# Kernel tuning notes

Measured on AMD Instinct MI355X. Metric: run time of the kernel, lower is better.

## Reference

```python
import jax, jax.numpy as jnp
import numpy as np

K = 20
EPS = 1e-5
NEG_SLOPE = 0.2


def _knn_idx(x, k):
    # x: (B, N, C). Torch: pd = -||xi||^2 + 2 xi.xj - ||xj||^2, topk largest = nearest.
    inner = jnp.einsum('bnc,bmc->bnm', x, x)
    xx = jnp.sum(x * x, axis=-1)  # (B, N)
    pd = 2.0 * inner - xx[:, :, None] - xx[:, None, :]
    _, idx = jax.lax.top_k(pd, k)  # (B, N, k)
    return idx


def _bn_lrelu(h, gamma, beta, axes):
    mean = jnp.mean(h, axis=axes)
    var = jnp.var(h, axis=axes)  # biased, as in torch BN training normalization
    hn = (h - mean) * jax.lax.rsqrt(var + EPS) * gamma + beta
    return jnp.where(hn >= 0, hn, NEG_SLOPE * hn)


def _edge_conv(x, W, gamma, beta, k):
    # x: (B, N, C); W: (O, 2C). Returns (B, N, O).
    idx = _knn_idx(x, k)
    nbr = jax.vmap(lambda xb, ib: xb[ib])(x, idx)  # (B, N, k, C) gather
    center = jnp.broadcast_to(x[:, :, None, :], nbr.shape)
    edge = jnp.concatenate([nbr - center, center], axis=-1)  # (B, N, k, 2C)
    h = jnp.einsum('bnkc,oc->bnko', edge, W)
    h = _bn_lrelu(h, gamma, beta, axes=(0, 1, 2))
    return jnp.max(h, axis=2)  # max over k -> (B, N, O)


def setup_inputs() -> dict:
    key = jax.random.key(0)
    ks = jax.random.split(key, 16)
    B, N = 32, 1024
    d = {'x': jax.random.normal(ks[0], (B, N, 3), dtype=jnp.float32)}
    dims = [(64, 6), (64, 128), (128, 128), (256, 256), (1024, 512)]
    for i, (o, c) in enumerate(dims, start=1):
        d[f'W{i}'] = jax.random.normal(ks[i], (o, c), dtype=jnp.float32) * 0.05
        d[f'g{i}'] = jnp.ones((o,), dtype=jnp.float32)
        d[f'b{i}'] = jnp.zeros((o,), dtype=jnp.float32)
    return d


def reference(x, W1, g1, b1, W2, g2, b2, W3, g3, b3, W4, g4, b4, W5, g5, b5):
    B = x.shape[0]
    x1 = _edge_conv(x, W1, g1, b1, K)    # (B, N, 64)
    x2 = _edge_conv(x1, W2, g2, b2, K)   # (B, N, 64)
    x3 = _edge_conv(x2, W3, g3, b3, K)   # (B, N, 128)
    x4 = _edge_conv(x3, W4, g4, b4, K)   # (B, N, 256)
    cat = jnp.concatenate([x1, x2, x3, x4], axis=-1)  # (B, N, 512)
    h = jnp.einsum('bnc,oc->bno', cat, W5)            # (B, N, 1024)
    h = _bn_lrelu(h, g5, b5, axes=(0, 1))
    out = jnp.max(h, axis=1)  # adaptive max pool over points -> (B, 1024)
    return out.reshape(B, 1, -1)
```

## Files before the change

kernel.cpp:

```cpp
#include <hip/hip_runtime.h>
#include <math.h>

#define BB 32
#define NN 1024
#define KNNK 20
#define PTS (BB*NN)

typedef __attribute__((ext_vector_type(8)))  short short8;
typedef __attribute__((ext_vector_type(4)))  float f32x4;
typedef __attribute__((ext_vector_type(16))) float f32x16;

__device__ __forceinline__ float lrelu(float v){ return v >= 0.f ? v : 0.2f*v; }

__device__ __forceinline__ unsigned short f2b(float x){
    union { float f; unsigned u; } c; c.f = x;
    unsigned r = c.u + 0x7FFFu + ((c.u >> 16) & 1u);
    return (unsigned short)(r >> 16);
}

__global__ void sq_kernel(const float* __restrict__ x, int stride, int C, float* __restrict__ xx){
    int pn = blockIdx.x*256 + threadIdx.x;
    if (pn >= PTS) return;
    const float* r = x + (size_t)pn*stride;
    float s = 0.f;
    for (int c = 0; c < C; ++c){ float v = r[c]; s = fmaf(v, v, s); }
    xx[pn] = s;
}

template<int C>
__global__ void __launch_bounds__(256) dist_kernel(const float* __restrict__ x, int stride,
                                                   const float* __restrict__ xx,
                                                   float* __restrict__ D, int b0){
    constexpr int KC = (C < 32 ? C : 32);
    __shared__ float As[KC][132];
    __shared__ float Bs[KC][132];
    const int tid = threadIdx.x;
    int t = blockIdx.x, ti = 0;
    while (t >= 8 - ti){ t -= 8 - ti; ++ti; }
    const int tj = ti + t;
    const int i0 = ti*128, j0 = tj*128;
    const int bl = blockIdx.z;
    const int b  = b0 + bl;
    const float* xb = x + (size_t)b*NN*stride;
    const int rt = tid >> 4, ct = tid & 15;
    float acc[8][8] = {{0.f}};

    for (int kc = 0; kc < C; kc += KC){
        __syncthreads();
        if constexpr (KC % 4 == 0){
            for (int i = tid; i < 128*(KC/4); i += 256){
                int kq = i % (KC/4), rr = i / (KC/4);
                float4 va = *(const float4*)&xb[(size_t)(i0+rr)*stride + kc + kq*4];
                As[kq*4+0][rr]=va.x; As[kq*4+1][rr]=va.y; As[kq*4+2][rr]=va.z; As[kq*4+3][rr]=va.w;
                float4 vb = *(const float4*)&xb[(size_t)(j0+rr)*stride + kc + kq*4];
                Bs[kq*4+0][rr]=vb.x; Bs[kq*4+1][rr]=vb.y; Bs[kq*4+2][rr]=vb.z; Bs[kq*4+3][rr]=vb.w;
            }
        } else {
            for (int i = tid; i < 128*KC; i += 256){
                int k = i % KC, rr = i / KC;
                As[k][rr] = xb[(size_t)(i0+rr)*stride + kc + k];
                Bs[k][rr] = xb[(size_t)(j0+rr)*stride + kc + k];
            }
        }
        __syncthreads();
        #pragma unroll
        for (int k = 0; k < KC; ++k){
            float4 a0 = *(const float4*)&As[k][rt*8];
            float4 a1 = *(const float4*)&As[k][rt*8+4];
            float4 b0v= *(const float4*)&Bs[k][ct*8];
            float4 b1v= *(const float4*)&Bs[k][ct*8+4];
            float av[8]={a0.x,a0.y,a0.z,a0.w,a1.x,a1.y,a1.z,a1.w};
            float bw[8]={b0v.x,b0v.y,b0v.z,b0v.w,b1v.x,b1v.y,b1v.z,b1v.w};
            #pragma unroll
            for (int i = 0; i < 8; ++i)
                #pragma unroll
                for (int j = 0; j < 8; ++j)
                    acc[i][j] = fmaf(av[i], bw[j], acc[i][j]);
        }
    }
    const float* xxb = xx + b*NN;
    float xi[8], xj[8];
    #pragma unroll
    for (int i=0;i<8;++i) xi[i] = xxb[i0 + rt*8 + i];
    #pragma unroll
    for (int j=0;j<8;++j) xj[j] = xxb[j0 + ct*8 + j];
    #pragma unroll
    for (int i=0;i<8;++i){
        float4 d0, d1;
        d0.x = 2.f*acc[i][0] - xi[i] - xj[0];
        d0.y = 2.f*acc[i][1] - xi[i] - xj[1];
        d0.z = 2.f*acc[i][2] - xi[i] - xj[2];
        d0.w = 2.f*acc[i][3] - xi[i] - xj[3];
        d1.x = 2.f*acc[i][4] - xi[i] - xj[4];
        d1.y = 2.f*acc[i][5] - xi[i] - xj[5];
        d1.z = 2.f*acc[i][6] - xi[i] - xj[6];
        d1.w = 2.f*acc[i][7] - xi[i] - xj[7];
        float* drow = &D[((size_t)bl*NN + i0 + rt*8 + i)*NN + j0 + ct*8];
        *(float4*)drow = d0;
        *(float4*)(drow+4) = d1;
    }
    if (ti != tj){
        #pragma unroll
        for (int j=0;j<8;++j){
            float4 m0, m1;
            m0.x = 2.f*acc[0][j] - xj[j] - xi[0];
            m0.y = 2.f*acc[1][j] - xj[j] - xi[1];
            m0.z = 2.f*acc[2][j] - xj[j] - xi[2];
            m0.w = 2.f*acc[3][j] - xj[j] - xi[3];
            m1.x = 2.f*acc[4][j] - xj[j] - xi[4];
            m1.y = 2.f*acc[5][j] - xj[j] - xi[5];
            m1.z = 2.f*acc[6][j] - xj[j] - xi[6];
            m1.w = 2.f*acc[7][j] - xj[j] - xi[7];
            float* mrow = &D[((size_t)bl*NN + j0 + ct*8 + j)*NN + i0 + rt*8];
            *(float4*)mrow = m0;
            *(float4*)(mrow+4) = m1;
        }
    }
}

__global__ void __launch_bounds__(256) topk_kernel(const float* __restrict__ D,
                                                   int* __restrict__ idxout, int baseRow){
    const int tid = threadIdx.x;
    const int wv = tid >> 6, lane = tid & 63;
    const int rid = blockIdx.x*4 + wv;
    const float* drow = D + (size_t)rid * NN;
    unsigned u[16];
    #pragma unroll
    for (int i = 0; i < 16; ++i){
        unsigned bits = __float_as_uint(drow[i*64 + lane]);
        unsigned m = (bits & 0x80000000u) ? 0xFFFFFFFFu : 0x80000000u;
        u[i] = bits ^ m;
    }
    unsigned t = 0u;
    for (int b = 31; b >= 0; --b){
        unsigned cand = t | (1u << b);
        int cnt = 0;
        #pragma unroll
        for (int i = 0; i < 16; ++i)
            cnt += (int)__popcll(__ballot(u[i] >= cand));
        if (cnt >= KNNK) t = cand;
    }
    const unsigned long long lt = (lane == 0) ? 0ull : ((~0ull) >> (64 - lane));
    int* orow = idxout + ((size_t)baseRow + rid) * KNNK;
    int cbase = 0;
    #pragma unroll
    for (int i = 0; i < 16; ++i){
        bool gt2 = (u[i] > t);
        unsigned long long mask = __ballot(gt2);
        if (gt2) orow[cbase + (int)__popcll(mask & lt)] = i*64 + lane;
        cbase += (int)__popcll(mask);
    }
    #pragma unroll
    for (int i = 0; i < 16; ++i){
        bool eq = (u[i] == t);
        unsigned long long mask = __ballot(eq);
        int pos = cbase + (int)__popcll(mask & lt);
        if (eq && pos < KNNK) orow[pos] = i*64 + lane;
        cbase += (int)__popcll(mask);
    }
}

template<int C, int O>
__global__ void __launch_bounds__(256) gemmG_kernel(const float* __restrict__ x, int stride,
                                                    const float* __restrict__ W,
                                                    float* __restrict__ G1, float* __restrict__ Gd){
    constexpr int KC = (C < 32 ? C : 32);
    __shared__ float Xl [KC][68];
    __shared__ float W1l[KC][68];
    __shared__ float W2l[KC][68];
    const int tid = threadIdx.x;
    const int r0 = blockIdx.x * 64;
    const int o0 = blockIdx.y * 64;
    const int rt = tid & 15, ct = tid >> 4;

    float a1[4][4] = {{0.f}}, a2[4][4] = {{0.f}};
    for (int kc = 0; kc < C; kc += KC){
        __syncthreads();
        for (int i = tid; i < KC*64; i += 256){
            int k = i % KC, rr = i / KC;
            Xl [k][rr] = x[(size_t)(r0+rr)*stride + kc + k];
            W1l[k][rr] = W[(size_t)(o0+rr)*(2*C) + kc + k];
            W2l[k][rr] = W[(size_t)(o0+rr)*(2*C) + C + kc + k];
        }
        __syncthreads();
        #pragma unroll
        for (int k = 0; k < KC; ++k){
            float4 xa = *(const float4*)&Xl [k][rt*4];
            float4 w1 = *(const float4*)&W1l[k][ct*4];
            float4 w2 = *(const float4*)&W2l[k][ct*4];
            float xv[4] = {xa.x, xa.y, xa.z, xa.w};
            #pragma unroll
            for (int i = 0; i < 4; ++i){
                a1[i][0] = fmaf(xv[i], w1.x, a1[i][0]);
                a1[i][1] = fmaf(xv[i], w1.y, a1[i][1]);
                a1[i][2] = fmaf(xv[i], w1.z, a1[i][2]);
                a1[i][3] = fmaf(xv[i], w1.w, a1[i][3]);
                a2[i][0] = fmaf(xv[i], w2.x, a2[i][0]);
                a2[i][1] = fmaf(xv[i], w2.y, a2[i][1]);
                a2[i][2] = fmaf(xv[i], w2.z, a2[i][2]);
                a2[i][3] = fmaf(xv[i], w2.w, a2[i][3]);
            }
        }
    }
    #pragma unroll
    for (int i = 0; i < 4; ++i){
        size_t row = (size_t)(r0 + rt*4 + i);
        float4 g1v = make_float4(a1[i][0], a1[i][1], a1[i][2], a1[i][3]);
        float4 gdv = make_float4(a2[i][0]-a1[i][0], a2[i][1]-a1[i][1],
                                 a2[i][2]-a1[i][2], a2[i][3]-a1[i][3]);
        *(float4*)&G1[row*O + o0 + ct*4] = g1v;
        *(float4*)&Gd[row*O + o0 + ct*4] = gdv;
    }
}

template<int O>
__global__ void __launch_bounds__(256) gather_kernel(const float* __restrict__ G1,
                                                     const float* __restrict__ Gd,
                                                     const int* __restrict__ idxg, int bgbase,
                                                     float* __restrict__ catslice,
                                                     float* __restrict__ stats){
    constexpr int OG = O/4;
    constexpr int PP = 256/OG;
    constexpr int NP = 16;
    __shared__ int nbs[NP][KNNK];
    const int nwg = (int)gridDim.x;
    int bid = (int)blockIdx.x;
    if ((nwg & 7) == 0){
        const int cpx = nwg >> 3;
        bid = (bid & 7) * cpx + (bid >> 3);
    }
    const int tid = threadIdx.x;
    const int p0 = bid * NP;
    for (int i = tid; i < NP*KNNK; i += 256){
        int pp = i / KNNK, kk = i - pp*KNNK;
        int pl = p0 + pp;
        nbs[pp][kk] = ((pl >> 10) << 10) + idxg[(size_t)(bgbase + pl)*KNNK + kk];
    }
    __syncthreads();
    const int o4 = (tid % OG)*4;
    const int pq = tid / OG;
    float S1[4] = {0.f,0.f,0.f,0.f}, S2[4] = {0.f,0.f,0.f,0.f};
    for (int pp = pq; pp < NP; pp += PP){
        int pl = p0 + pp;
        float4 dv = *(const float4*)&Gd[(size_t)pl*O + o4];
        float d[4] = {dv.x, dv.y, dv.z, dv.w};
        float mx[4] = {-INFINITY,-INFINITY,-INFINITY,-INFINITY};
        float ls[4] = {0.f,0.f,0.f,0.f}, lq[4] = {0.f,0.f,0.f,0.f};
        #pragma unroll
        for (int kk = 0; kk < KNNK; ++kk){
            float4 gv = *(const float4*)&G1[(size_t)nbs[pp][kk]*O + o4];
            float ga[4] = {gv.x, gv.y, gv.z, gv.w};
            #pragma unroll
            for (int c = 0; c < 4; ++c){
                mx[c] = fmaxf(mx[c], ga[c]);
                ls[c] += ga[c];
                lq[c] = fmaf(ga[c], ga[c], lq[c]);
            }
        }
        float4 outv;
        float* op = &outv.x;
        #pragma unroll
        for (int c = 0; c < 4; ++c){
            S1[c] += ls[c] + 20.f*d[c];
            S2[c] += lq[c] + 2.f*d[c]*ls[c] + 20.f*d[c]*d[c];
            op[c] = mx[c] + d[c];
        }
        *(float4*)&catslice[(size_t)(bgbase + pl)*512 + o4] = outv;
    }
    int rep = bid & 63;
    #pragma unroll
    for (int c = 0; c < 4; ++c){
        atomicAdd(&stats[rep*2*O + o4 + c],     S1[c]);
        atomicAdd(&stats[rep*2*O + O + o4 + c], S2[c]);
    }
}

__global__ void fin_kernel(const float* __restrict__ stats, int O, float cnt,
                           float* __restrict__ mean, float* __restrict__ invstd){
    int o = threadIdx.x;
    if (o >= O) return;
    float s1 = 0.f, s2 = 0.f;
    for (int r = 0; r < 64; ++r){
        s1 += stats[r*2*O + o];
        s2 += stats[r*2*O + O + o];
    }
    float m = s1 / cnt;
    float v = s2 / cnt - m*m;
    mean[o] = m;
    invstd[o] = rsqrtf(v + 1e-5f);
}

template<int O>
__global__ void apply_kernel(float* __restrict__ catslice,
                             const float* __restrict__ mean, const float* __restrict__ invstd,
                             const float* __restrict__ g, const float* __restrict__ bt){
    int i = blockIdx.x*256 + threadIdx.x;
    int pn = i / O, o = i - pn*O;
    float* p = &catslice[(size_t)pn*512 + o];
    float hn = (*p - mean[o]) * invstd[o] * g[o] + bt[o];
    *p = lrelu(hn);
}

__global__ void tob16_kernel(const float* __restrict__ src, unsigned short* __restrict__ dst, int n4){
    int i = blockIdx.x*256 + threadIdx.x;
    if (i >= n4) return;
    float4 v = *(const float4*)&src[(size_t)i*4];
    ushort4 o;
    o.x = f2b(v.x); o.y = f2b(v.y); o.z = f2b(v.z); o.w = f2b(v.w);
    *(ushort4*)&dst[(size_t)i*4] = o;
}

__global__ void __launch_bounds__(256) l5m_kernel(const unsigned short* __restrict__ Am,
                                                  const unsigned short* __restrict__ Bm,
                                                  float* __restrict__ pmax,
                                                  float* __restrict__ psum,
                                                  float* __restrict__ psq){
    __shared__ __align__(16) unsigned short As[128][64];
    __shared__ __align__(16) unsigned short Bs[128][64];
    const int tid = threadIdx.x;
    const int r0 = blockIdx.x * 128;
    const int o0 = blockIdx.y * 128;
    const int w = tid >> 6, lane = tid & 63;
    const int m32 = lane & 31, kh = lane >> 5;
    const int wm = (w & 1) * 64;
    const int wn = (w >> 1) * 64;

    f32x16 acc[2][2];
    #pragma unroll
    for (int i=0;i<2;++i)
        #pragma unroll
        for (int j=0;j<2;++j)
            #pragma unroll
            for (int r=0;r<16;++r) acc[i][j][r] = 0.f;

    for (int kc = 0; kc < 512; kc += 64){
        __syncthreads();
        #pragma unroll
        for (int t = 0; t < 4; ++t){
            int i = tid + t*256;
            int rr = i >> 3, ch = i & 7;
            int sl = ch ^ (rr & 7);
            *(uint4*)&As[rr][sl*8] = *(const uint4*)&Am[(size_t)(r0+rr)*512 + kc + ch*8];
            *(uint4*)&Bs[rr][sl*8] = *(const uint4*)&Bm[(size_t)(o0+rr)*512 + kc + ch*8];
        }
        __syncthreads();
        #pragma unroll
        for (int q = 0; q < 4; ++q){
            int lk = q*2 + kh;
            short8 a[2], bfr[2];
            #pragma unroll
            for (int mb = 0; mb < 2; ++mb){
                int rA = wm + mb*32 + m32;
                a[mb] = *(const short8*)&As[rA][(lk ^ (rA & 7))*8];
            }
            #pragma unroll
            for (int nb = 0; nb < 2; ++nb){
                int rB = wn + nb*32 + m32;
                bfr[nb] = *(const short8*)&Bs[rB][(lk ^ (rB & 7))*8];
            }
            #pragma unroll
            for (int mb = 0; mb < 2; ++mb)
                #pragma unroll
                for (int nb = 0; nb < 2; ++nb)
                    acc[mb][nb] = __builtin_amdgcn_mfma_f32_32x32x16_bf16(a[mb], bfr[nb], acc[mb][nb], 0, 0, 0);
        }
    }
    __syncthreads();
    float* red = (float*)&As[0][0];
    #pragma unroll
    for (int nb = 0; nb < 2; ++nb){
        float mx = -INFINITY, s1 = 0.f, s2 = 0.f;
        #pragma unroll
        for (int mb = 0; mb < 2; ++mb)
            #pragma unroll
            for (int r = 0; r < 16; ++r){
                float v = acc[mb][nb][r];
                mx = fmaxf(mx, v); s1 += v; s2 = fmaf(v, v, s2);
            }
        mx = fmaxf(mx, __shfl_xor(mx, 32));
        s1 += __shfl_xor(s1, 32);
        s2 += __shfl_xor(s2, 32);
        if (lane < 32){
            int col = wn + nb*32 + m32;
            float* p = red + ((size_t)(w & 1) * 128 + col) * 3;
            p[0] = mx; p[1] = s1; p[2] = s2;
        }
    }
    __syncthreads();
    if (tid < 128){
        const float* p0 = red + (size_t)tid*3;
        const float* p1 = red + (size_t)(128 + tid)*3;
        float mx = fmaxf(p0[0], p1[0]);
        float s1 = p0[1] + p1[1];
        float s2 = p0[2] + p1[2];
        size_t pi = (size_t)blockIdx.x*1024 + o0 + tid;
        pmax[pi] = mx; psum[pi] = s1; psq[pi] = s2;
    }
}

__global__ void fin5_kernel(const float* __restrict__ pmax, const float* __restrict__ psum,
                            const float* __restrict__ psq,
                            const float* __restrict__ g, const float* __restrict__ bt,
                            float* __restrict__ out){
    int o = blockIdx.x*256 + threadIdx.x;
    float s1 = 0.f, s2 = 0.f;
    for (int r = 0; r < 256; ++r){
        s1 += psum[(size_t)r*1024 + o];
        s2 += psq [(size_t)r*1024 + o];
    }
    float m  = s1 / 32768.f;
    float v  = s2 / 32768.f - m*m;
    float is = rsqrtf(v + 1e-5f);
    float gg = g[o], bb2 = bt[o];
    for (int b = 0; b < 32; ++b){
        float mx = -INFINITY;
        #pragma unroll
        for (int ns = 0; ns < 8; ++ns) mx = fmaxf(mx, pmax[((size_t)b*8 + ns)*1024 + o]);
        float hn = (mx - m) * is * gg + bb2;
        out[(size_t)b*1024 + o] = lrelu(hn);
    }
}

extern "C" void kernel_launch(void* const* d_in, const int* in_sizes, int n_in,
                              void* d_out, int out_size, void* d_ws, size_t ws_size,
                              hipStream_t stream) {
    (void)in_sizes; (void)n_in; (void)out_size;
    const float* x  = (const float*)d_in[0];
    const float* W1 = (const float*)d_in[1];  const float* g1 = (const float*)d_in[2];  const float* b1 = (const float*)d_in[3];
    const float* W2 = (const float*)d_in[4];  const float* g2 = (const float*)d_in[5];  const float* b2 = (const float*)d_in[6];
    const float* W3 = (const float*)d_in[7];  const float* g3 = (const float*)d_in[8];  const float* b3 = (const float*)d_in[9];
    const float* W4 = (const float*)d_in[10]; const float* g4 = (const float*)d_in[11]; const float* b4 = (const float*)d_in[12];
    const float* W5 = (const float*)d_in[13]; const float* g5 = (const float*)d_in[14]; const float* b5 = (const float*)d_in[15];
    float* out = (float*)d_out;

    const size_t fixedBytes = (size_t)PTS*512*4 + (size_t)PTS*KNNK*4 + (size_t)PTS*4
                            + (size_t)64*2*256*4 + 2048*4 + 3*(size_t)256*1024*4
                            + (size_t)1024*512*2;
    int CB;
    if      (ws_size >= fixedBytes + (size_t)32*NN*NN*4) CB = 32;
    else if (ws_size >= fixedBytes + (size_t)16*NN*NN*4) CB = 16;
    else                                                 CB = 8;
    const size_t Rbytes = (size_t)CB*NN*NN*4;

    char* wsp = (char*)d_ws;
    float* cat    = (float*)wsp; wsp += (size_t)PTS*512*4;
    char*  R      = wsp;         wsp += Rbytes;
    int*   idx    = (int*)  wsp; wsp += (size_t)PTS*KNNK*4;
    float* xx     = (float*)wsp; wsp += (size_t)PTS*4;
    float* stats  = (float*)wsp; wsp += (size_t)64*2*256*4;
    float* mean   = (float*)wsp; wsp += 1024*4;
    float* invstd = (float*)wsp; wsp += 1024*4;
    float* pmax   = (float*)wsp; wsp += (size_t)256*1024*4;
    float* psum   = (float*)wsp; wsp += (size_t)256*1024*4;
    float* psq    = (float*)wsp; wsp += (size_t)256*1024*4;
    unsigned short* W5b = (unsigned short*)wsp; wsp += (size_t)1024*512*2;

    float* Dbuf  = (float*)R;
    float* G1    = (float*)R;
    float* GdS   = (float*)(R + (size_t)16*1024*1024);
    float* GdB   = (float*)(R + (size_t)32*1024*1024);
    unsigned short* catB = (unsigned short*)R;

    const float cntE = (float)(PTS*KNNK);
    const int nch = 32 / CB;
    const bool bigG = (Rbytes >= (size_t)64*1024*1024);

    sq_kernel<<<PTS/256, 256, 0, stream>>>(x, 3, 3, xx);
    for (int bc = 0; bc < nch; ++bc){
        dist_kernel<3><<<dim3(36,1,CB), 256, 0, stream>>>(x, 3, xx, Dbuf, bc*CB);
        topk_kernel<<<CB*1024/4, 256, 0, stream>>>(Dbuf, idx, bc*CB*1024);
    }
    hipMemsetAsync(stats, 0, 64*2*256*4, stream);
    gemmG_kernel<3,64><<<dim3(512,1), 256, 0, stream>>>(x, 3, W1, G1, GdS);
    gather_kernel<64><<<2048, 256, 0, stream>>>(G1, GdS, idx, 0, cat + 0, stats);
    fin_kernel<<<1, 64, 0, stream>>>(stats, 64, cntE, mean, invstd);
    apply_kernel<64><<<PTS*64/256, 256, 0, stream>>>(cat + 0, mean, invstd, g1, b1);

    sq_kernel<<<PTS/256, 256, 0, stream>>>(cat + 0, 512, 64, xx);
    for (int bc = 0; bc < nch; ++bc){
        dist_kernel<64><<<dim3(36,1,CB), 256, 0, stream>>>(cat + 0, 512, xx, Dbuf, bc*CB);
        topk_kernel<<<CB*1024/4, 256, 0, stream>>>(Dbuf, idx, bc*CB*1024);
    }
    hipMemsetAsync(stats, 0, 64*2*256*4, stream);
    gemmG_kernel<64,64><<<dim3(512,1), 256, 0, stream>>>(cat + 0, 512, W2, G1, GdS);
    gather_kernel<64><<<2048, 256, 0, stream>>>(G1, GdS, idx, 0, cat + 64, stats);
    fin_kernel<<<1, 64, 0, stream>>>(stats, 64, cntE, mean, invstd);
    apply_kernel<64><<<PTS*64/256, 256, 0, stream>>>(cat + 64, mean, invstd, g2, b2);

    sq_kernel<<<PTS/256, 256, 0, stream>>>(cat + 64, 512, 64, xx);
    for (int bc = 0; bc < nch; ++bc){
        dist_kernel<64><<<dim3(36,1,CB), 256, 0, stream>>>(cat + 64, 512, xx, Dbuf, bc*CB);
        topk_kernel<<<CB*1024/4, 256, 0, stream>>>(Dbuf, idx, bc*CB*1024);
    }
    hipMemsetAsync(stats, 0, 64*2*256*4, stream);
    gemmG_kernel<64,128><<<dim3(512,2), 256, 0, stream>>>(cat + 64, 512, W3, G1, GdS);
    gather_kernel<128><<<2048, 256, 0, stream>>>(G1, GdS, idx, 0, cat + 128, stats);
    fin_kernel<<<1, 128, 0, stream>>>(stats, 128, cntE, mean, invstd);
    apply_kernel<128><<<PTS*128/256, 256, 0, stream>>>(cat + 128, mean, invstd, g3, b3);

    sq_kernel<<<PTS/256, 256, 0, stream>>>(cat + 128, 512, 128, xx);
    for (int bc = 0; bc < nch; ++bc){
        dist_kernel<128><<<dim3(36,1,CB), 256, 0, stream>>>(cat + 128, 512, xx, Dbuf, bc*CB);
        topk_kernel<<<CB*1024/4, 256, 0, stream>>>(Dbuf, idx, bc*CB*1024);
    }
    hipMemsetAsync(stats, 0, 64*2*256*4, stream);
    if (bigG){
        gemmG_kernel<128,256><<<dim3(512,4), 256, 0, stream>>>(cat + 128, 512, W4, G1, GdB);
        gather_kernel<256><<<2048, 256, 0, stream>>>(G1, GdB, idx, 0, cat + 256, stats);
    } else {
        for (int bg = 0; bg < 4; ++bg){
            gemmG_kernel<128,256><<<dim3(128,4), 256, 0, stream>>>(cat + 128 + (size_t)bg*8192*512, 512, W4, G1, GdS);
            gather_kernel<256><<<512, 256, 0, stream>>>(G1, GdS, idx, bg*8192, cat + 256, stats);
        }
    }
    fin_kernel<<<1, 256, 0, stream>>>(stats, 256, cntE, mean, invstd);
    apply_kernel<256><<<PTS*256/256, 256, 0, stream>>>(cat + 256, mean, invstd, g4, b4);

    tob16_kernel<<<PTS*512/4/256, 256, 0, stream>>>(cat, catB, PTS*512/4);
    tob16_kernel<<<1024*512/4/256, 256, 0, stream>>>(W5, W5b, 1024*512/4);
    l5m_kernel<<<dim3(256, 8), 256, 0, stream>>>(catB, W5b, pmax, psum, psq);
    fin5_kernel<<<4, 256, 0, stream>>>(pmax, psum, psq, g5, b5, out);
}
```

Measured before the change: 1.204 ms.

## Fuse pairwise distance and top-k selection into one kNN kernel

Measured after the change: 3.133 ms. +160.1%, slower.

```diff
diff --git a/kernel.cpp b/kernel.cpp
--- a/kernel.cpp
+++ b/kernel.cpp
@@ -28,135 +28,118 @@
 }
 
 template<int C>
-__global__ void __launch_bounds__(256) dist_kernel(const float* __restrict__ x, int stride,
-                                                   const float* __restrict__ xx,
-                                                   float* __restrict__ D, int b0){
-    constexpr int KC = (C < 32 ? C : 32);
-    __shared__ float As[KC][132];
-    __shared__ float Bs[KC][132];
-    const int tid = threadIdx.x;
-    int t = blockIdx.x, ti = 0;
-    while (t >= 8 - ti){ t -= 8 - ti; ++ti; }
-    const int tj = ti + t;
-    const int i0 = ti*128, j0 = tj*128;
-    const int bl = blockIdx.z;
-    const int b  = b0 + bl;
-    const float* xb = x + (size_t)b*NN*stride;
-    const int rt = tid >> 4, ct = tid & 15;
-    float acc[8][8] = {{0.f}};
-
-    for (int kc = 0; kc < C; kc += KC){
-        __syncthreads();
-        if constexpr (KC % 4 == 0){
-            for (int i = tid; i < 128*(KC/4); i += 256){
-                int kq = i % (KC/4), rr = i / (KC/4);
-                float4 va = *(const float4*)&xb[(size_t)(i0+rr)*stride + kc + kq*4];
-                As[kq*4+0][rr]=va.x; As[kq*4+1][rr]=va.y; As[kq*4+2][rr]=va.z; As[kq*4+3][rr]=va.w;
-                float4 vb = *(const float4*)&xb[(size_t)(j0+rr)*stride + kc + kq*4];
-                Bs[kq*4+0][rr]=vb.x; Bs[kq*4+1][rr]=vb.y; Bs[kq*4+2][rr]=vb.z; Bs[kq*4+3][rr]=vb.w;
-            }
-        } else {
-            for (int i = tid; i < 128*KC; i += 256){
-                int k = i % KC, rr = i / KC;
-                As[k][rr] = xb[(size_t)(i0+rr)*stride + kc + k];
-                Bs[k][rr] = xb[(size_t)(j0+rr)*stride + kc + k];
-            }
-        }
-        __syncthreads();
-        #pragma unroll
-        for (int k = 0; k < KC; ++k){
-            float4 a0 = *(const float4*)&As[k][rt*8];
-            float4 a1 = *(const float4*)&As[k][rt*8+4];
-            float4 b0v= *(const float4*)&Bs[k][ct*8];
-            float4 b1v= *(const float4*)&Bs[k][ct*8+4];
-            float av[8]={a0.x,a0.y,a0.z,a0.w,a1.x,a1.y,a1.z,a1.w};
-            float bw[8]={b0v.x,b0v.y,b0v.z,b0v.w,b1v.x,b1v.y,b1v.z,b1v.w};
-            #pragma unroll
-            for (int i = 0; i < 8; ++i)
-                #pragma unroll
-                for (int j = 0; j < 8; ++j)
-                    acc[i][j] = fmaf(av[i], bw[j], acc[i][j]);
-        }
-    }
-    const float* xxb = xx + b*NN;
-    float xi[8], xj[8];
-    #pragma unroll
-    for (int i=0;i<8;++i) xi[i] = xxb[i0 + rt*8 + i];
-    #pragma unroll
-    for (int j=0;j<8;++j) xj[j] = xxb[j0 + ct*8 + j];
-    #pragma unroll
-    for (int i=0;i<8;++i){
-        float4 d0, d1;
-        d0.x = 2.f*acc[i][0] - xi[i] - xj[0];
-        d0.y = 2.f*acc[i][1] - xi[i] - xj[1];
-        d0.z = 2.f*acc[i][2] - xi[i] - xj[2];
-        d0.w = 2.f*acc[i][3] - xi[i] - xj[3];
-        d1.x = 2.f*acc[i][4] - xi[i] - xj[4];
-        d1.y = 2.f*acc[i][5] - xi[i] - xj[5];
-        d1.z = 2.f*acc[i][6] - xi[i] - xj[6];
-        d1.w = 2.f*acc[i][7] - xi[i] - xj[7];
-        float* drow = &D[((size_t)bl*NN + i0 + rt*8 + i)*NN + j0 + ct*8];
-        *(float4*)drow = d0;
-        *(float4*)(drow+4) = d1;
-    }
-    if (ti != tj){
-        #pragma unroll
-        for (int j=0;j<8;++j){
-            float4 m0, m1;
-            m0.x = 2.f*acc[0][j] - xj[j] - xi[0];
-            m0.y = 2.f*acc[1][j] - xj[j] - xi[1];
-            m0.z = 2.f*acc[2][j] - xj[j] - xi[2];
-            m0.w = 2.f*acc[3][j] - xj[j] - xi[3];
-            m1.x = 2.f*acc[4][j] - xj[j] - xi[4];
-            m1.y = 2.f*acc[5][j] - xj[j] - xi[5];
-            m1.z = 2.f*acc[6][j] - xj[j] - xi[6];
-            m1.w = 2.f*acc[7][j] - xj[j] - xi[7];
-            float* mrow = &D[((size_t)bl*NN + j0 + ct*8 + j)*NN + i0 + rt*8];
-            *(float4*)mrow = m0;
-            *(float4*)(mrow+4) = m1;
-        }
-    }
-}
-
-__global__ void __launch_bounds__(256) topk_kernel(const float* __restrict__ D,
-                                                   int* __restrict__ idxout, int baseRow){
+__global__ void __launch_bounds__(256, 2) knn_kernel(const float* __restrict__ x, int stride,
+                                                     const float* __restrict__ xx,
+                                                     int* __restrict__ idxout){
+    constexpr int KC = 8;
+    __shared__ __align__(16) float Bs[NN*KC];
+    __shared__ float xs[NN];
+    int bid = (int)blockIdx.x;
+    bid = (bid & 7)*128 + (bid >> 3);
+    const int b  = bid >> 5;
+    const int rb = bid & 31;
+    const int r0 = rb * 32;
     const int tid = threadIdx.x;
     const int wv = tid >> 6, lane = tid & 63;
-    const int rid = blockIdx.x*4 + wv;
-    const float* drow = D + (size_t)rid * NN;
-    unsigned u[16];
+    const float* xb = x + (size_t)b*NN*stride;
+
+    *(float4*)&xs[tid*4] = *(const float4*)&xx[b*NN + tid*4];
+
+    float acc[8][16];
     #pragma unroll
-    for (int i = 0; i < 16; ++i){
-        unsigned bits = __float_as_uint(drow[i*64 + lane]);
-        unsigned m = (bits & 0x80000000u) ? 0xFFFFFFFFu : 0x80000000u;
-        u[i] = bits ^ m;
-    }
-    unsigned t = 0u;
-    for (int b = 31; b >= 0; --b){
-        unsigned cand = t | (1u << b);
-        int cnt = 0;
-        #pragma unroll
-        for (int i = 0; i < 16; ++i)
-            cnt += (int)__popcll(__ballot(u[i] >= cand));
-        if (cnt >= KNNK) t = cand;
-    }
+    for (int r=0;r<8;++r)
+        #pragma unroll
+        for (int q=0;q<16;++q) acc[r][q] = 0.f;
+
+    const int wrow = wv*8;
+    const int swl  = (lane>>2)&1;
+
+    #pragma unroll 1
+    for (int kc = 0; kc < C; kc += KC){
+        __syncthreads();
+        #pragma unroll
+        for (int ps = 0; ps < 8; ++ps){
+            int i = tid + ps*256;
+            int col = i >> 1, half = i & 1;
+            float4 v;
+            if constexpr (C == 3){
+                float vv[4];
+                #pragma unroll
+                for (int j = 0; j < 4; ++j){
+                    int k = half*4 + j;
+                    vv[j] = (k < 3) ? xb[(size_t)col*3 + k] : 0.f;
+                }
+                v = make_float4(vv[0], vv[1], vv[2], vv[3]);
+            } else {
+                v = *(const float4*)&xb[(size_t)col*stride + kc + half*4];
+            }
+            int sw = half ^ ((col>>2)&1);
+            *(float4*)&Bs[col*KC + sw*4] = v;
+        }
+        __syncthreads();
+        #pragma unroll
+        for (int s = 0; s < 2; ++s){
+            float4 ar[8];
+            #pragma unroll
+            for (int r=0;r<8;++r){
+                int arow = r0 + wrow + r;
+                int swa = s ^ ((arow>>2)&1);
+                ar[r] = *(const float4*)&Bs[arow*KC + swa*4];
+            }
+            int offb = (s ^ swl)*4;
+            #pragma unroll
+            for (int q=0;q<16;++q){
+                float4 bv = *(const float4*)&Bs[(lane + 64*q)*KC + offb];
+                #pragma unroll
+                for (int r=0;r<8;++r){
+                    acc[r][q] = fmaf(ar[r].x, bv.x, acc[r][q]);
+                    acc[r][q] = fmaf(ar[r].y, bv.y, acc[r][q]);
+                    acc[r][q] = fmaf(ar[r].z, bv.z, acc[r][q]);
+                    acc[r][q] = fmaf(ar[r].w, bv.w, acc[r][q]);
+                }
+            }
+        }
+    }
+
     const unsigned long long lt = (lane == 0) ? 0ull : ((~0ull) >> (64 - lane));
-    int* orow = idxout + ((size_t)baseRow + rid) * KNNK;
-    int cbase = 0;
-    #pragma unroll
-    for (int i = 0; i < 16; ++i){
-        bool gt2 = (u[i] > t);
-        unsigned long long mask = __ballot(gt2);
-        if (gt2) orow[cbase + (int)__popcll(mask & lt)] = i*64 + lane;
-        cbase += (int)__popcll(mask);
-    }
-    #pragma unroll
-    for (int i = 0; i < 16; ++i){
-        bool eq = (u[i] == t);
-        unsigned long long mask = __ballot(eq);
-        int pos = cbase + (int)__popcll(mask & lt);
-        if (eq && pos < KNNK) orow[pos] = i*64 + lane;
-        cbase += (int)__popcll(mask);
+    #pragma unroll 1
+    for (int r = 0; r < 8; ++r){
+        const int lrow = r0 + wrow + r;
+        const float xi = xs[lrow];
+        unsigned u[16];
+        #pragma unroll
+        for (int q = 0; q < 16; ++q){
+            float d = 2.f*acc[r][q] - xi - xs[lane + 64*q];
+            unsigned bits = __float_as_uint(d);
+            unsigned m = (bits & 0x80000000u) ? 0xFFFFFFFFu : 0x80000000u;
+            u[q] = bits ^ m;
+        }
+        unsigned t = 0u;
+        for (int bb = 31; bb >= 0; --bb){
+            unsigned cand = t | (1u << bb);
+            int cnt = 0;
+            #pragma unroll
+            for (int q = 0; q < 16; ++q)
+                cnt += (int)__popcll(__ballot(u[q] >= cand));
+            if (cnt >= KNNK) t = cand;
+        }
+        int* orow = idxout + ((size_t)b*NN + lrow) * KNNK;
+        int cbase = 0;
+        #pragma unroll
+        for (int q = 0; q < 16; ++q){
+            bool gt2 = (u[q] > t);
+            unsigned long long mask = __ballot(gt2);
+            if (gt2) orow[cbase + (int)__popcll(mask & lt)] = q*64 + lane;
+            cbase += (int)__popcll(mask);
+        }
+        #pragma unroll
+        for (int q = 0; q < 16; ++q){
+            bool eq = (u[q] == t);
+            unsigned long long mask = __ballot(eq);
+            int pos = cbase + (int)__popcll(mask & lt);
+            if (eq && pos < KNNK) orow[pos] = q*64 + lane;
+            cbase += (int)__popcll(mask);
+        }
     }
 }
 
@@ -455,21 +438,16 @@
     float* psq    = (float*)wsp; wsp += (size_t)256*1024*4;
     unsigned short* W5b = (unsigned short*)wsp; wsp += (size_t)1024*512*2;
 
-    float* Dbuf  = (float*)R;
     float* G1    = (float*)R;
     float* GdS   = (float*)(R + (size_t)16*1024*1024);
     float* GdB   = (float*)(R + (size_t)32*1024*1024);
     unsigned short* catB = (unsigned short*)R;
 
     const float cntE = (float)(PTS*KNNK);
-    const int nch = 32 / CB;
     const bool bigG = (Rbytes >= (size_t)64*1024*1024);
 
     sq_kernel<<<PTS/256, 256, 0, stream>>>(x, 3, 3, xx);
-    for (int bc = 0; bc < nch; ++bc){
-        dist_kernel<3><<<dim3(36,1,CB), 256, 0, stream>>>(x, 3, xx, Dbuf, bc*CB);
-        topk_kernel<<<CB*1024/4, 256, 0, stream>>>(Dbuf, idx, bc*CB*1024);
-    }
+    knn_kernel<3><<<1024, 256, 0, stream>>>(x, 3, xx, idx);
     hipMemsetAsync(stats, 0, 64*2*256*4, stream);
     gemmG_kernel<3,64><<<dim3(512,1), 256, 0, stream>>>(x, 3, W1, G1, GdS);
     gather_kernel<64><<<2048, 256, 0, stream>>>(G1, GdS, idx, 0, cat + 0, stats);
@@ -477,10 +455,7 @@
     apply_kernel<64><<<PTS*64/256, 256, 0, stream>>>(cat + 0, mean, invstd, g1, b1);
 
     sq_kernel<<<PTS/256, 256, 0, stream>>>(cat + 0, 512, 64, xx);
-    for (int bc = 0; bc < nch; ++bc){
-        dist_kernel<64><<<dim3(36,1,CB), 256, 0, stream>>>(cat + 0, 512, xx, Dbuf, bc*CB);
-        topk_kernel<<<CB*1024/4, 256, 0, stream>>>(Dbuf, idx, bc*CB*1024);
-    }
+    knn_kernel<64><<<1024, 256, 0, stream>>>(cat + 0, 512, xx, idx);
     hipMemsetAsync(stats, 0, 64*2*256*4, stream);
     gemmG_kernel<64,64><<<dim3(512,1), 256, 0, stream>>>(cat + 0, 512, W2, G1, GdS);
     gather_kernel<64><<<2048, 256, 0, stream>>>(G1, GdS, idx, 0, cat + 64, stats);
@@ -488,10 +463,7 @@
     apply_kernel<64><<<PTS*64/256, 256, 0, stream>>>(cat + 64, mean, invstd, g2, b2);
 
     sq_kernel<<<PTS/256, 256, 0, stream>>>(cat + 64, 512, 64, xx);
-    for (int bc = 0; bc < nch; ++bc){
-        dist_kernel<64><<<dim3(36,1,CB), 256, 0, stream>>>(cat + 64, 512, xx, Dbuf, bc*CB);
-        topk_kernel<<<CB*1024/4, 256, 0, stream>>>(Dbuf, idx, bc*CB*1024);
-    }
+    knn_kernel<64><<<1024, 256, 0, stream>>>(cat + 64, 512, xx, idx);
     hipMemsetAsync(stats, 0, 64*2*256*4, stream);
     gemmG_kernel<64,128><<<dim3(512,2), 256, 0, stream>>>(cat + 64, 512, W3, G1, GdS);
     gather_kernel<128><<<2048, 256, 0, stream>>>(G1, GdS, idx, 0, cat + 128, stats);
@@ -499,10 +471,7 @@
     apply_kernel<128><<<PTS*128/256, 256, 0, stream>>>(cat + 128, mean, invstd, g3, b3);
 
     sq_kernel<<<PTS/256, 256, 0, stream>>>(cat + 128, 512, 128, xx);
-    for (int bc = 0; bc < nch; ++bc){
-        dist_kernel<128><<<dim3(36,1,CB), 256, 0, stream>>>(cat + 128, 512, xx, Dbuf, bc*CB);
-        topk_kernel<<<CB*1024/4, 256, 0, stream>>>(Dbuf, idx, bc*CB*1024);
-    }
+    knn_kernel<128><<<1024, 256, 0, stream>>>(cat + 128, 512, xx, idx);
     hipMemsetAsync(stats, 0, 64*2*256*4, stream);
     if (bigG){
         gemmG_kernel<128,256><<<dim3(512,4), 256, 0, stream>>>(cat + 128, 512, W4, G1, GdB);
```
